# Kernel optimization log

Hardware: AMD Instinct MI355X
Metric: run time of the kernel (lower is better)

## Reference

```python
import jax, jax.numpy as jnp
import numpy as np

C_PAIR = 128
N_TOK = 512
EPS = 1e-5


def _layernorm(x, w, b):
    mu = jnp.mean(x, axis=-1, keepdims=True)
    var = jnp.mean(jnp.square(x - mu), axis=-1, keepdims=True)
    return (x - mu) * jax.lax.rsqrt(var + EPS) * w + b


def setup_inputs() -> dict:
    key = jax.random.key(0)
    ks = jax.random.split(key, 8)
    c = C_PAIR
    pair = jax.random.normal(ks[0], (N_TOK, N_TOK, c), dtype=jnp.float32)
    mask = jax.random.uniform(ks[1], (N_TOK, N_TOK), dtype=jnp.float32)
    s_in = 1.0 / np.sqrt(c)
    W_proj = jax.random.normal(ks[2], (2 * c, c), dtype=jnp.float32) * s_in  # nn.Linear(c, 2c)
    W_gate = jax.random.normal(ks[3], (2 * c, c), dtype=jnp.float32) * s_in
    W_out = jax.random.normal(ks[4], (c, c), dtype=jnp.float32) * s_in
    W_glin = jax.random.normal(ks[5], (c, c), dtype=jnp.float32) * s_in
    ln1_w = jnp.ones((c,), jnp.float32)
    ln1_b = jnp.zeros((c,), jnp.float32)
    ln2_w = jnp.ones((c,), jnp.float32)
    ln2_b = jnp.zeros((c,), jnp.float32)
    return {"pair": pair, "mask": mask, "ln1_w": ln1_w, "ln1_b": ln1_b,
            "ln2_w": ln2_w, "ln2_b": ln2_b, "W_proj": W_proj, "W_gate": W_gate,
            "W_out": W_out, "W_glin": W_glin}


def reference(pair, mask, ln1_w, ln1_b, ln2_w, ln2_b, W_proj, W_gate, W_out, W_glin):
    # pair: [N, N, c], mask: [N, N]
    x = _layernorm(pair, ln1_w, ln1_b)
    input_pair = x
    proj = x @ W_proj.T                      # [N, N, 2c]
    proj = proj * mask[..., None]
    gate = x @ W_gate.T                      # [N, N, 2c]
    proj = proj * jax.nn.sigmoid(gate)
    # torch reshape(2c,...)->(c,2,...) then chunk: a = channels 0::2, b = channels 1::2
    a = proj[..., 0::2]                      # [N, N, c]
    b = proj[..., 1::2]                      # [N, N, c]
    # equation 'ckj,cki->cij' in channel-first == out[i,j,c] = sum_k a[k,j,c] * b[k,i,c]
    out = jnp.einsum('kjc,kic->ijc', a, b)   # [N, N, c]
    out = _layernorm(out, ln2_w, ln2_b)
    out = out @ W_out.T
    gate_out = input_pair @ W_glin.T
    return out * jax.nn.sigmoid(gate_out)
```

## Files before the change

### kernel.cpp

```cpp
#include <hip/hip_runtime.h>
#include <hip/hip_bf16.h>

using u16 = unsigned short;
typedef __attribute__((ext_vector_type(4))) float f32x4;
typedef __attribute__((ext_vector_type(8))) short s16x8;
typedef __attribute__((ext_vector_type(4))) unsigned short u16x4;

#define MFMA(a,b,c) __builtin_amdgcn_mfma_f32_16x16x32_bf16((a),(b),(c),0,0,0)

__device__ __forceinline__ u16 f2bf(float f){
  unsigned u = __builtin_bit_cast(unsigned, f);
  u += 0x7fff + ((u >> 16) & 1);
  return (u16)(u >> 16);
}
__device__ __forceinline__ float bf2f(u16 h){
  unsigned u = ((unsigned)h) << 16;
  return __builtin_bit_cast(float, u);
}
__device__ __forceinline__ float sigm(float x){
  return 1.f / (1.f + __expf(-x));
}

__global__ void k0_prep(const float* __restrict__ Wp, const float* __restrict__ Wg,
                        const float* __restrict__ Wgl, const float* __restrict__ Wo,
                        u16* __restrict__ Wc, u16* __restrict__ WoB){
  int idx = blockIdx.x * 256 + threadIdx.x;
  if (idx < 640 * 128){
    int n = idx >> 7, k = idx & 127;
    float v;
    if (n < 256)      v = Wp[n * 128 + k];
    else if (n < 512) v = Wg[(n - 256) * 128 + k];
    else              v = Wgl[(n - 512) * 128 + k];
    Wc[idx] = f2bf(v);
  }
  if (idx < 128 * 128) WoB[idx] = f2bf(Wo[idx]);
}

__launch_bounds__(256, 2)
__global__ void k1_ln_proj(const float* __restrict__ pair, const float* __restrict__ mask,
                           const float* __restrict__ ln1w, const float* __restrict__ ln1b,
                           const u16* __restrict__ Wc,
                           u16* __restrict__ a_r, u16* __restrict__ b_r, u16* __restrict__ g){
  __shared__ float red_s[128], red_q[128], msk[128];
  __shared__ u16 xs[128 * 136];
  int tid = threadIdx.x;
  int bid = blockIdx.x;
  int j   = bid >> 2;
  int k0  = (bid & 3) << 7;

  int cpos = tid & 31;
  int rsub = tid >> 5;
  float4 v[16];
  #pragma unroll
  for (int it = 0; it < 16; ++it){
    int kk = it * 8 + rsub;
    const float4* p = (const float4*)(pair + (((size_t)(k0 + kk) * 512 + j) << 7));
    v[it] = p[cpos];
    float s = v[it].x + v[it].y + v[it].z + v[it].w;
    float q = v[it].x*v[it].x + v[it].y*v[it].y + v[it].z*v[it].z + v[it].w*v[it].w;
    #pragma unroll
    for (int m = 16; m >= 1; m >>= 1){
      s += __shfl_xor(s, m);
      q += __shfl_xor(q, m);
    }
    if (cpos == 0){ red_s[kk] = s; red_q[kk] = q; }
  }
  if (tid < 128) msk[tid] = mask[(size_t)(k0 + tid) * 512 + j];
  __syncthreads();

  float4 w4 = ((const float4*)ln1w)[cpos];
  float4 b4 = ((const float4*)ln1b)[cpos];
  #pragma unroll
  for (int it = 0; it < 16; ++it){
    int kk = it * 8 + rsub;
    float mu = red_s[kk] * (1.f / 128.f);
    float var = red_q[kk] * (1.f / 128.f) - mu * mu;
    float rs = rsqrtf(var + 1e-5f);
    u16x4 o;
    o[0] = f2bf((v[it].x - mu) * rs * w4.x + b4.x);
    o[1] = f2bf((v[it].y - mu) * rs * w4.y + b4.y);
    o[2] = f2bf((v[it].z - mu) * rs * w4.z + b4.z);
    o[3] = f2bf((v[it].w - mu) * rs * w4.w + b4.w);
    *(u16x4*)&xs[kk * 136 + cpos * 4] = o;
  }
  __syncthreads();

  int lane = tid & 63;
  int wv   = tid >> 6;
  int l15  = lane & 15;
  int l4   = lane >> 4;

  for (int pi = 0; pi < 4; ++pi){
    int tp = pi * 4 + wv;
    int nP = tp * 16 + l15;
    f32x4 accP[8] = {}; f32x4 accG[8] = {};
    #pragma unroll
    for (int ks = 0; ks < 4; ++ks){
      s16x8 bP = *(const s16x8*)&Wc[nP * 128 + ks * 32 + l4 * 8];
      s16x8 bG = *(const s16x8*)&Wc[(256 + nP) * 128 + ks * 32 + l4 * 8];
      #pragma unroll
      for (int mi = 0; mi < 8; ++mi){
        s16x8 af = *(const s16x8*)&xs[(mi * 16 + l15) * 136 + ks * 32 + l4 * 8];
        accP[mi] = MFMA(af, bP, accP[mi]);
        accG[mi] = MFMA(af, bG, accG[mi]);
      }
    }
    int c = nP >> 1;
    u16* dst = (nP & 1) ? b_r : a_r;
    #pragma unroll
    for (int mi = 0; mi < 8; ++mi){
      int m0 = mi * 16 + l4 * 4;
      u16x4 o;
      #pragma unroll
      for (int r = 0; r < 4; ++r){
        float p = accP[mi][r] * msk[m0 + r] * sigm(accG[mi][r]);
        o[r] = f2bf(p);
      }
      *(u16x4*)&dst[((size_t)c * 512 + j) * 512 + k0 + m0] = o;
    }
  }

  for (int gi = 0; gi < 2; ++gi){
    int tg = gi * 4 + wv;
    int cg = tg * 16 + l15;
    f32x4 acc[8] = {};
    #pragma unroll
    for (int ks = 0; ks < 4; ++ks){
      s16x8 bW = *(const s16x8*)&Wc[(512 + cg) * 128 + ks * 32 + l4 * 8];
      #pragma unroll
      for (int mi = 0; mi < 8; ++mi){
        s16x8 af = *(const s16x8*)&xs[(mi * 16 + l15) * 136 + ks * 32 + l4 * 8];
        acc[mi] = MFMA(af, bW, acc[mi]);
      }
    }
    #pragma unroll
    for (int mi = 0; mi < 8; ++mi){
      int m0 = mi * 16 + l4 * 4;
      #pragma unroll
      for (int r = 0; r < 4; ++r){
        g[(((size_t)(k0 + m0 + r) * 512 + j) << 7) + cg] = f2bf(sigm(acc[mi][r]));
      }
    }
  }
}

__launch_bounds__(256, 2)
__global__ void k2_tri(const u16* __restrict__ a_r, const u16* __restrict__ b_r,
                       u16* __restrict__ out_r){
  int tid = threadIdx.x, bid = blockIdx.x;
  int c  = bid >> 4;
  int t  = bid & 15;
  int lane = tid & 63, wv = tid >> 6;
  int i0 = (t >> 2) * 128 + (wv >> 1) * 64;
  int j0 = (t & 3) * 128 + (wv & 1) * 64;
  int l15 = lane & 15, l4 = lane >> 4;
  const u16* pa = a_r + (size_t)c * 262144;
  const u16* pb = b_r + (size_t)c * 262144;

  f32x4 acc[4][4] = {};
  for (int ks = 0; ks < 16; ++ks){
    s16x8 A[4], B[4];
    #pragma unroll
    for (int ai = 0; ai < 4; ++ai)
      A[ai] = *(const s16x8*)&pb[(i0 + ai * 16 + l15) * 512 + ks * 32 + l4 * 8];
    #pragma unroll
    for (int bj = 0; bj < 4; ++bj)
      B[bj] = *(const s16x8*)&pa[(j0 + bj * 16 + l15) * 512 + ks * 32 + l4 * 8];
    #pragma unroll
    for (int ai = 0; ai < 4; ++ai)
      #pragma unroll
      for (int bj = 0; bj < 4; ++bj)
        acc[ai][bj] = MFMA(A[ai], B[bj], acc[ai][bj]);
  }
  u16* po = out_r + (size_t)c * 262144;
  #pragma unroll
  for (int ai = 0; ai < 4; ++ai){
    #pragma unroll
    for (int r = 0; r < 4; ++r){
      int i = i0 + ai * 16 + l4 * 4 + r;
      #pragma unroll
      for (int bj = 0; bj < 4; ++bj)
        po[i * 512 + j0 + bj * 16 + l15] = f2bf(acc[ai][bj][r]);
    }
  }
}

__launch_bounds__(256, 2)
__global__ void k3_out(const u16* __restrict__ out_r, const u16* __restrict__ g,
                       const float* __restrict__ ln2w, const float* __restrict__ ln2b,
                       const u16* __restrict__ WoB, float* __restrict__ out){
  __shared__ u16 ot[128 * 72];
  __shared__ u16 x2[64 * 136];
  int tid = threadIdx.x, bid = blockIdx.x;
  int i  = bid >> 3;
  int j0 = (bid & 7) << 6;

  #pragma unroll
  for (int it = 0; it < 8; ++it){
    int f = it * 256 + tid;
    int cin = f >> 4, part = f & 15;
    u16x4 vld = *(const u16x4*)&out_r[(size_t)cin * 262144 + i * 512 + j0 + part * 4];
    *(u16x4*)&ot[cin * 72 + part * 4] = vld;
  }
  __syncthreads();

  int jj = tid >> 2, qr = tid & 3;
  float s = 0.f, q = 0.f;
  #pragma unroll
  for (int u = 0; u < 32; ++u){
    float x = bf2f(ot[(qr * 32 + u) * 72 + jj]);
    s += x; q += x * x;
  }
  s += __shfl_xor(s, 1); q += __shfl_xor(q, 1);
  s += __shfl_xor(s, 2); q += __shfl_xor(q, 2);
  float mu = s * (1.f / 128.f);
  float rs = rsqrtf(q * (1.f / 128.f) - mu * mu + 1e-5f);
  #pragma unroll
  for (int u = 0; u < 32; ++u){
    int cin = qr * 32 + u;
    float x = bf2f(ot[cin * 72 + jj]);
    x2[jj * 136 + cin] = f2bf((x - mu) * rs * ln2w[cin] + ln2b[cin]);
  }
  __syncthreads();

  int lane = tid & 63, wv = tid >> 6;
  int l15 = lane & 15, l4 = lane >> 4;
  int n0 = wv * 32;
  f32x4 acc[4][2] = {};
  #pragma unroll
  for (int ks = 0; ks < 4; ++ks){
    s16x8 B0 = *(const s16x8*)&WoB[(n0 + l15) * 128 + ks * 32 + l4 * 8];
    s16x8 B1 = *(const s16x8*)&WoB[(n0 + 16 + l15) * 128 + ks * 32 + l4 * 8];
    #pragma unroll
    for (int mi = 0; mi < 4; ++mi){
      s16x8 A = *(const s16x8*)&x2[(mi * 16 + l15) * 136 + ks * 32 + l4 * 8];
      acc[mi][0] = MFMA(A, B0, acc[mi][0]);
      acc[mi][1] = MFMA(A, B1, acc[mi][1]);
    }
  }
  #pragma unroll
  for (int mi = 0; mi < 4; ++mi){
    #pragma unroll
    for (int r = 0; r < 4; ++r){
      int m = mi * 16 + l4 * 4 + r;
      size_t tok = (size_t)i * 512 + j0 + m;
      #pragma unroll
      for (int nj = 0; nj < 2; ++nj){
        int cout = n0 + nj * 16 + l15;
        float gv = bf2f(g[tok * 128 + cout]);
        out[tok * 128 + cout] = acc[mi][nj][r] * gv;
      }
    }
  }
}

extern "C" void kernel_launch(void* const* d_in, const int* in_sizes, int n_in,
                              void* d_out, int out_size, void* d_ws, size_t ws_size,
                              hipStream_t stream){
  (void)in_sizes; (void)n_in; (void)out_size; (void)ws_size;
  const float* pair = (const float*)d_in[0];
  const float* mask = (const float*)d_in[1];
  const float* ln1w = (const float*)d_in[2];
  const float* ln1b = (const float*)d_in[3];
  const float* ln2w = (const float*)d_in[4];
  const float* ln2b = (const float*)d_in[5];
  const float* Wp   = (const float*)d_in[6];
  const float* Wg   = (const float*)d_in[7];
  const float* Wo   = (const float*)d_in[8];
  const float* Wgl  = (const float*)d_in[9];
  float* out = (float*)d_out;

  char* ws = (char*)d_ws;
  u16* a_r = (u16*)(ws);
  u16* b_r = (u16*)(ws + 67108864);
  u16* g   = (u16*)(ws + 134217728);
  u16* o_r = (u16*)(ws + 201326592);
  u16* Wc  = (u16*)(ws + 268435456);
  u16* WoB = (u16*)(ws + 268435456 + 163840);

  hipLaunchKernelGGL(k0_prep,   dim3(320),  dim3(256), 0, stream, Wp, Wg, Wgl, Wo, Wc, WoB);
  hipLaunchKernelGGL(k1_ln_proj,dim3(2048), dim3(256), 0, stream, pair, mask, ln1w, ln1b, Wc, a_r, b_r, g);
  hipLaunchKernelGGL(k2_tri,    dim3(2048), dim3(256), 0, stream, a_r, b_r, o_r);
  hipLaunchKernelGGL(k3_out,    dim3(4096), dim3(256), 0, stream, o_r, g, ln2w, ln2b, WoB, out);
}
```

Before: 404.2 us.

## Recompute output gate in final kernel, switch to fp16 MFMA, stage projection stores

Removes the weight-prep kernel by converting fp32 weights to fp16 on the fly inside the GEMM kernels. The gate-linear branch moves from k1 into k3, which re-reads pair and recomputes layernorm1, so the 64MB gate tensor is never written or read back. The a/b projection stores are staged through LDS for coalesced writes. k2 now writes fp32 output instead of bf16, and block order is swizzled. Everything switches from bf16 to fp16 MFMA, which risks overflow range issues, and the fp32 intermediate doubles that tensor's traffic.

```diff
diff --git a/kernel.cpp b/kernel.cpp
--- a/kernel.cpp
+++ b/kernel.cpp
@@ -3,46 +3,35 @@
 
 using u16 = unsigned short;
 typedef __attribute__((ext_vector_type(4))) float f32x4;
-typedef __attribute__((ext_vector_type(8))) short s16x8;
+typedef __attribute__((ext_vector_type(8))) _Float16 f16x8;
 typedef __attribute__((ext_vector_type(4))) unsigned short u16x4;
 
-#define MFMA(a,b,c) __builtin_amdgcn_mfma_f32_16x16x32_bf16((a),(b),(c),0,0,0)
-
-__device__ __forceinline__ u16 f2bf(float f){
-  unsigned u = __builtin_bit_cast(unsigned, f);
-  u += 0x7fff + ((u >> 16) & 1);
-  return (u16)(u >> 16);
-}
-__device__ __forceinline__ float bf2f(u16 h){
-  unsigned u = ((unsigned)h) << 16;
-  return __builtin_bit_cast(float, u);
+#define MFMA(a,b,c) __builtin_amdgcn_mfma_f32_16x16x32_f16((a),(b),(c),0,0,0)
+
+__device__ __forceinline__ u16 f2h(float f){
+  _Float16 h = (_Float16)f;
+  return __builtin_bit_cast(u16, h);
 }
 __device__ __forceinline__ float sigm(float x){
   return 1.f / (1.f + __expf(-x));
 }
-
-__global__ void k0_prep(const float* __restrict__ Wp, const float* __restrict__ Wg,
-                        const float* __restrict__ Wgl, const float* __restrict__ Wo,
-                        u16* __restrict__ Wc, u16* __restrict__ WoB){
-  int idx = blockIdx.x * 256 + threadIdx.x;
-  if (idx < 640 * 128){
-    int n = idx >> 7, k = idx & 127;
-    float v;
-    if (n < 256)      v = Wp[n * 128 + k];
-    else if (n < 512) v = Wg[(n - 256) * 128 + k];
-    else              v = Wgl[(n - 512) * 128 + k];
-    Wc[idx] = f2bf(v);
-  }
-  if (idx < 128 * 128) WoB[idx] = f2bf(Wo[idx]);
-}
-
-__launch_bounds__(256, 2)
+__device__ __forceinline__ f16x8 ldw8(const float* __restrict__ W, int row, int koff){
+  const float4* p = (const float4*)(W + row * 128 + koff);
+  float4 f0 = p[0], f1 = p[1];
+  f16x8 h;
+  h[0] = (_Float16)f0.x; h[1] = (_Float16)f0.y; h[2] = (_Float16)f0.z; h[3] = (_Float16)f0.w;
+  h[4] = (_Float16)f1.x; h[5] = (_Float16)f1.y; h[6] = (_Float16)f1.z; h[7] = (_Float16)f1.w;
+  return h;
+}
+
+__launch_bounds__(256, 3)
 __global__ void k1_ln_proj(const float* __restrict__ pair, const float* __restrict__ mask,
                            const float* __restrict__ ln1w, const float* __restrict__ ln1b,
-                           const u16* __restrict__ Wc,
-                           u16* __restrict__ a_r, u16* __restrict__ b_r, u16* __restrict__ g){
+                           const float* __restrict__ Wp, const float* __restrict__ Wg,
+                           u16* __restrict__ a_r, u16* __restrict__ b_r){
   __shared__ float red_s[128], red_q[128], msk[128];
   __shared__ u16 xs[128 * 136];
+  __shared__ u16 sbuf[4][16 * 132];
   int tid = threadIdx.x;
   int bid = blockIdx.x;
   int j   = bid >> 2;
@@ -77,10 +66,10 @@
     float var = red_q[kk] * (1.f / 128.f) - mu * mu;
     float rs = rsqrtf(var + 1e-5f);
     u16x4 o;
-    o[0] = f2bf((v[it].x - mu) * rs * w4.x + b4.x);
-    o[1] = f2bf((v[it].y - mu) * rs * w4.y + b4.y);
-    o[2] = f2bf((v[it].z - mu) * rs * w4.z + b4.z);
-    o[3] = f2bf((v[it].w - mu) * rs * w4.w + b4.w);
+    o[0] = f2h((v[it].x - mu) * rs * w4.x + b4.x);
+    o[1] = f2h((v[it].y - mu) * rs * w4.y + b4.y);
+    o[2] = f2h((v[it].z - mu) * rs * w4.z + b4.z);
+    o[3] = f2h((v[it].w - mu) * rs * w4.w + b4.w);
     *(u16x4*)&xs[kk * 136 + cpos * 4] = o;
   }
   __syncthreads();
@@ -89,24 +78,24 @@
   int wv   = tid >> 6;
   int l15  = lane & 15;
   int l4   = lane >> 4;
-
+  u16* sb  = sbuf[wv];
+
+  #pragma unroll
   for (int pi = 0; pi < 4; ++pi){
     int tp = pi * 4 + wv;
     int nP = tp * 16 + l15;
     f32x4 accP[8] = {}; f32x4 accG[8] = {};
     #pragma unroll
     for (int ks = 0; ks < 4; ++ks){
-      s16x8 bP = *(const s16x8*)&Wc[nP * 128 + ks * 32 + l4 * 8];
-      s16x8 bG = *(const s16x8*)&Wc[(256 + nP) * 128 + ks * 32 + l4 * 8];
+      f16x8 bP = ldw8(Wp, nP, ks * 32 + l4 * 8);
+      f16x8 bG = ldw8(Wg, nP, ks * 32 + l4 * 8);
       #pragma unroll
       for (int mi = 0; mi < 8; ++mi){
-        s16x8 af = *(const s16x8*)&xs[(mi * 16 + l15) * 136 + ks * 32 + l4 * 8];
+        f16x8 af = *(const f16x8*)&xs[(mi * 16 + l15) * 136 + ks * 32 + l4 * 8];
         accP[mi] = MFMA(af, bP, accP[mi]);
         accG[mi] = MFMA(af, bG, accG[mi]);
       }
     }
-    int c = nP >> 1;
-    u16* dst = (nP & 1) ? b_r : a_r;
     #pragma unroll
     for (int mi = 0; mi < 8; ++mi){
       int m0 = mi * 16 + l4 * 4;
@@ -114,42 +103,31 @@
       #pragma unroll
       for (int r = 0; r < 4; ++r){
         float p = accP[mi][r] * msk[m0 + r] * sigm(accG[mi][r]);
-        o[r] = f2bf(p);
+        o[r] = f2h(p);
       }
-      *(u16x4*)&dst[((size_t)c * 512 + j) * 512 + k0 + m0] = o;
-    }
-  }
-
-  for (int gi = 0; gi < 2; ++gi){
-    int tg = gi * 4 + wv;
-    int cg = tg * 16 + l15;
-    f32x4 acc[8] = {};
-    #pragma unroll
-    for (int ks = 0; ks < 4; ++ks){
-      s16x8 bW = *(const s16x8*)&Wc[(512 + cg) * 128 + ks * 32 + l4 * 8];
-      #pragma unroll
-      for (int mi = 0; mi < 8; ++mi){
-        s16x8 af = *(const s16x8*)&xs[(mi * 16 + l15) * 136 + ks * 32 + l4 * 8];
-        acc[mi] = MFMA(af, bW, acc[mi]);
-      }
-    }
-    #pragma unroll
-    for (int mi = 0; mi < 8; ++mi){
-      int m0 = mi * 16 + l4 * 4;
-      #pragma unroll
-      for (int r = 0; r < 4; ++r){
-        g[(((size_t)(k0 + m0 + r) * 512 + j) << 7) + cg] = f2bf(sigm(acc[mi][r]));
-      }
+      *(u16x4*)&sb[l15 * 132 + m0] = o;
+    }
+    #pragma unroll
+    for (int r2 = 0; r2 < 8; ++r2){
+      int row = r2 * 2 + (lane >> 5);
+      int col = (lane & 31) * 4;
+      u16x4 vv = *(const u16x4*)&sb[row * 132 + col];
+      int nP2 = tp * 16 + row;
+      int c = nP2 >> 1;
+      u16* dst = (nP2 & 1) ? b_r : a_r;
+      *(u16x4*)&dst[((size_t)c * 512 + j) * 512 + k0 + col] = vv;
     }
   }
 }
 
 __launch_bounds__(256, 2)
 __global__ void k2_tri(const u16* __restrict__ a_r, const u16* __restrict__ b_r,
-                       u16* __restrict__ out_r){
-  int tid = threadIdx.x, bid = blockIdx.x;
-  int c  = bid >> 4;
-  int t  = bid & 15;
+                       float* __restrict__ o_f){
+  int tid = threadIdx.x;
+  int p = blockIdx.x;
+  int lb = (p & 7) * 256 + (p >> 3);
+  int c  = lb >> 4;
+  int t  = lb & 15;
   int lane = tid & 63, wv = tid >> 6;
   int i0 = (t >> 2) * 128 + (wv >> 1) * 64;
   int j0 = (t & 3) * 128 + (wv & 1) * 64;
@@ -159,20 +137,20 @@
 
   f32x4 acc[4][4] = {};
   for (int ks = 0; ks < 16; ++ks){
-    s16x8 A[4], B[4];
+    f16x8 A[4], B[4];
     #pragma unroll
     for (int ai = 0; ai < 4; ++ai)
-      A[ai] = *(const s16x8*)&pb[(i0 + ai * 16 + l15) * 512 + ks * 32 + l4 * 8];
+      A[ai] = *(const f16x8*)&pb[(i0 + ai * 16 + l15) * 512 + ks * 32 + l4 * 8];
     #pragma unroll
     for (int bj = 0; bj < 4; ++bj)
-      B[bj] = *(const s16x8*)&pa[(j0 + bj * 16 + l15) * 512 + ks * 32 + l4 * 8];
+      B[bj] = *(const f16x8*)&pa[(j0 + bj * 16 + l15) * 512 + ks * 32 + l4 * 8];
     #pragma unroll
     for (int ai = 0; ai < 4; ++ai)
       #pragma unroll
       for (int bj = 0; bj < 4; ++bj)
         acc[ai][bj] = MFMA(A[ai], B[bj], acc[ai][bj]);
   }
-  u16* po = out_r + (size_t)c * 262144;
+  float* po = o_f + (size_t)c * 262144;
   #pragma unroll
   for (int ai = 0; ai < 4; ++ai){
     #pragma unroll
@@ -180,62 +158,108 @@
       int i = i0 + ai * 16 + l4 * 4 + r;
       #pragma unroll
       for (int bj = 0; bj < 4; ++bj)
-        po[i * 512 + j0 + bj * 16 + l15] = f2bf(acc[ai][bj][r]);
+        po[i * 512 + j0 + bj * 16 + l15] = acc[ai][bj][r];
     }
   }
 }
 
 __launch_bounds__(256, 2)
-__global__ void k3_out(const u16* __restrict__ out_r, const u16* __restrict__ g,
+__global__ void k3_out(const float* __restrict__ o_f, const float* __restrict__ pair,
+                       const float* __restrict__ ln1w, const float* __restrict__ ln1b,
                        const float* __restrict__ ln2w, const float* __restrict__ ln2b,
-                       const u16* __restrict__ WoB, float* __restrict__ out){
-  __shared__ u16 ot[128 * 72];
+                       const float* __restrict__ Wgl, const float* __restrict__ Wo,
+                       float* __restrict__ out){
+  __shared__ float ot[128 * 68];
+  __shared__ u16 x1[64 * 136];
   __shared__ u16 x2[64 * 136];
+  __shared__ float r1s[64], r1q[64];
   int tid = threadIdx.x, bid = blockIdx.x;
   int i  = bid >> 3;
   int j0 = (bid & 7) << 6;
 
+  int cq = tid & 31, jsub = tid >> 5;
+  float4 pv[8];
+  #pragma unroll
+  for (int it = 0; it < 8; ++it){
+    int jj = it * 8 + jsub;
+    const float4* p = (const float4*)(pair + (((size_t)i * 512 + j0 + jj) << 7));
+    pv[it] = p[cq];
+    float s = pv[it].x + pv[it].y + pv[it].z + pv[it].w;
+    float q = pv[it].x*pv[it].x + pv[it].y*pv[it].y + pv[it].z*pv[it].z + pv[it].w*pv[it].w;
+    #pragma unroll
+    for (int m = 16; m >= 1; m >>= 1){
+      s += __shfl_xor(s, m);
+      q += __shfl_xor(q, m);
+    }
+    if (cq == 0){ r1s[jj] = s; r1q[jj] = q; }
+  }
+  __syncthreads();
+  {
+    float4 w1 = ((const float4*)ln1w)[cq];
+    float4 b1 = ((const float4*)ln1b)[cq];
+    #pragma unroll
+    for (int it = 0; it < 8; ++it){
+      int jj = it * 8 + jsub;
+      float mu = r1s[jj] * (1.f / 128.f);
+      float var = r1q[jj] * (1.f / 128.f) - mu * mu;
+      float rs = rsqrtf(var + 1e-5f);
+      u16x4 o;
+      o[0] = f2h((pv[it].x - mu) * rs * w1.x + b1.x);
+      o[1] = f2h((pv[it].y - mu) * rs * w1.y + b1.y);
+      o[2] = f2h((pv[it].z - mu) * rs * w1.z + b1.z);
+      o[3] = f2h((pv[it].w - mu) * rs * w1.w + b1.w);
+      *(u16x4*)&x1[jj * 136 + cq * 4] = o;
+    }
+  }
+
   #pragma unroll
   for (int it = 0; it < 8; ++it){
     int f = it * 256 + tid;
     int cin = f >> 4, part = f & 15;
-    u16x4 vld = *(const u16x4*)&out_r[(size_t)cin * 262144 + i * 512 + j0 + part * 4];
-    *(u16x4*)&ot[cin * 72 + part * 4] = vld;
-  }
-  __syncthreads();
-
-  int jj = tid >> 2, qr = tid & 3;
-  float s = 0.f, q = 0.f;
+    float4 vld = *(const float4*)&o_f[(size_t)cin * 262144 + (size_t)i * 512 + j0 + part * 4];
+    *(float4*)&ot[cin * 68 + part * 4] = vld;
+  }
+  __syncthreads();
+
+  int jj2 = tid >> 2, qr = tid & 3;
+  float s2 = 0.f, q2 = 0.f;
   #pragma unroll
   for (int u = 0; u < 32; ++u){
-    float x = bf2f(ot[(qr * 32 + u) * 72 + jj]);
-    s += x; q += x * x;
-  }
-  s += __shfl_xor(s, 1); q += __shfl_xor(q, 1);
-  s += __shfl_xor(s, 2); q += __shfl_xor(q, 2);
-  float mu = s * (1.f / 128.f);
-  float rs = rsqrtf(q * (1.f / 128.f) - mu * mu + 1e-5f);
+    float x = ot[(qr * 32 + u) * 68 + jj2];
+    s2 += x; q2 += x * x;
+  }
+  s2 += __shfl_xor(s2, 1); q2 += __shfl_xor(q2, 1);
+  s2 += __shfl_xor(s2, 2); q2 += __shfl_xor(q2, 2);
+  float mu2 = s2 * (1.f / 128.f);
+  float rs2 = rsqrtf(q2 * (1.f / 128.f) - mu2 * mu2 + 1e-5f);
   #pragma unroll
   for (int u = 0; u < 32; ++u){
     int cin = qr * 32 + u;
-    float x = bf2f(ot[cin * 72 + jj]);
-    x2[jj * 136 + cin] = f2bf((x - mu) * rs * ln2w[cin] + ln2b[cin]);
+    float x = ot[cin * 68 + jj2];
+    x2[jj2 * 136 + cin] = f2h((x - mu2) * rs2 * ln2w[cin] + ln2b[cin]);
   }
   __syncthreads();
 
   int lane = tid & 63, wv = tid >> 6;
   int l15 = lane & 15, l4 = lane >> 4;
   int n0 = wv * 32;
-  f32x4 acc[4][2] = {};
+  f32x4 accO[4][2] = {};
+  f32x4 accG[4][2] = {};
   #pragma unroll
   for (int ks = 0; ks < 4; ++ks){
-    s16x8 B0 = *(const s16x8*)&WoB[(n0 + l15) * 128 + ks * 32 + l4 * 8];
-    s16x8 B1 = *(const s16x8*)&WoB[(n0 + 16 + l15) * 128 + ks * 32 + l4 * 8];
+    int koff = ks * 32 + l4 * 8;
+    f16x8 B0 = ldw8(Wo, n0 + l15, koff);
+    f16x8 B1 = ldw8(Wo, n0 + 16 + l15, koff);
+    f16x8 G0 = ldw8(Wgl, n0 + l15, koff);
+    f16x8 G1 = ldw8(Wgl, n0 + 16 + l15, koff);
     #pragma unroll
     for (int mi = 0; mi < 4; ++mi){
-      s16x8 A = *(const s16x8*)&x2[(mi * 16 + l15) * 136 + ks * 32 + l4 * 8];
-      acc[mi][0] = MFMA(A, B0, acc[mi][0]);
-      acc[mi][1] = MFMA(A, B1, acc[mi][1]);
+      f16x8 A2 = *(const f16x8*)&x2[(mi * 16 + l15) * 136 + koff];
+      f16x8 A1 = *(const f16x8*)&x1[(mi * 16 + l15) * 136 + koff];
+      accO[mi][0] = MFMA(A2, B0, accO[mi][0]);
+      accO[mi][1] = MFMA(A2, B1, accO[mi][1]);
+      accG[mi][0] = MFMA(A1, G0, accG[mi][0]);
+      accG[mi][1] = MFMA(A1, G1, accG[mi][1]);
     }
   }
   #pragma unroll
@@ -247,8 +271,7 @@
       #pragma unroll
       for (int nj = 0; nj < 2; ++nj){
         int cout = n0 + nj * 16 + l15;
-        float gv = bf2f(g[tok * 128 + cout]);
-        out[tok * 128 + cout] = acc[mi][nj][r] * gv;
+        out[tok * 128 + cout] = accO[mi][nj][r] * sigm(accG[mi][nj][r]);
       }
     }
   }
@@ -271,15 +294,11 @@
   float* out = (float*)d_out;
 
   char* ws = (char*)d_ws;
-  u16* a_r = (u16*)(ws);
-  u16* b_r = (u16*)(ws + 67108864);
-  u16* g   = (u16*)(ws + 134217728);
-  u16* o_r = (u16*)(ws + 201326592);
-  u16* Wc  = (u16*)(ws + 268435456);
-  u16* WoB = (u16*)(ws + 268435456 + 163840);
-
-  hipLaunchKernelGGL(k0_prep,   dim3(320),  dim3(256), 0, stream, Wp, Wg, Wgl, Wo, Wc, WoB);
-  hipLaunchKernelGGL(k1_ln_proj,dim3(2048), dim3(256), 0, stream, pair, mask, ln1w, ln1b, Wc, a_r, b_r, g);
-  hipLaunchKernelGGL(k2_tri,    dim3(2048), dim3(256), 0, stream, a_r, b_r, o_r);
-  hipLaunchKernelGGL(k3_out,    dim3(4096), dim3(256), 0, stream, o_r, g, ln2w, ln2b, WoB, out);
-}
+  u16*   a_r = (u16*)(ws);
+  u16*   b_r = (u16*)(ws + 67108864);
+  float* o_f = (float*)(ws + 134217728);
+
+  hipLaunchKernelGGL(k1_ln_proj, dim3(2048), dim3(256), 0, stream, pair, mask, ln1w, ln1b, Wp, Wg, a_r, b_r);
+  hipLaunchKernelGGL(k2_tri,     dim3(2048), dim3(256), 0, stream, a_r, b_r, o_f);
+  hipLaunchKernelGGL(k3_out,     dim3(4096), dim3(256), 0, stream, o_f, pair, ln1w, ln1b, ln2w, ln2b, Wgl, Wo, out);
+}
```

After: 447.7 us. +10.8%, slower.
